# Kernel optimization log

Measured on AMD Instinct MI355X. Metric: run time of the kernel, lower is better.

## Reference

```python
import jax, jax.numpy as jnp
import numpy as np
import math

NEG = -10000.0  # module uses -10000, not -inf


def setup_inputs() -> dict:
    key = jax.random.key(0)
    k1, k2, k3 = jax.random.split(key, 3)
    B, Sq, Sk, H, Hkv, D = 2, 2048, 2048, 16, 4, 64
    q = jax.random.normal(k1, (B, Sq, H, D), dtype=jnp.float32)
    kv = jax.random.normal(k2, (B, Sk, 2, Hkv, D), dtype=jnp.float32)
    key_padding_mask = jax.random.randint(k3, (B, Sk), 0, 2) > 0  # True = valid key
    return {"q": q, "kv": kv, "key_padding_mask": key_padding_mask}


def reference(q, kv, key_padding_mask):
    B, Sq, H, D = q.shape
    Sk, Hkv = kv.shape[1], kv.shape[3]
    if Hkv != H:
        # einops repeat '... hkv d -> ... (hkv g) d': each kv head repeated g times contiguously
        kv = jnp.repeat(kv, H // Hkv, axis=3)
    k, v = kv[:, :, 0], kv[:, :, 1]  # [B, Sk, H, D] each
    scale = 1.0 / math.sqrt(D)
    scores = jnp.einsum('bthd,bshd->bhts', q, k * scale)  # [B, H, Sq, Sk]
    # key padding: additive 0 where valid, -10000 where padded
    pad = jnp.where(key_padding_mask, 0.0, NEG).astype(scores.dtype)
    scores = scores + pad[:, None, None, :]
    # causal mask: cols > rows + Sk - Sq gets replaced (not added) with -10000
    rows = jnp.arange(Sq)[:, None]
    cols = jnp.arange(Sk)[None, :]
    causal_mask = cols > rows + (Sk - Sq)
    scores = jnp.where(causal_mask, NEG, scores)
    attention = jax.nn.softmax(scores, axis=-1).astype(v.dtype)
    # dropout p=0.0 -> identity
    output = jnp.einsum('bhts,bshd->bthd', attention, v)  # [B, Sq, H, D]
    return output
```

## Files before the change

### kernel.cpp

```cpp
#include <hip/hip_runtime.h>
#include <math.h>


typedef __bf16 bf16x4 __attribute__((ext_vector_type(4)));
typedef __bf16 bf16x8 __attribute__((ext_vector_type(8)));
typedef float floatx4 __attribute__((ext_vector_type(4)));
typedef short shortx4 __attribute__((ext_vector_type(4)));

#define SQ 2048
#define SK 2048
#define H_ 16
#define HKV 4
#define D_ 64
#define QT 64
#define KT 64
#define KVROW 512
#define NEGV (-10000.0f)
#define QSCL 0.18033688f
#define EBIAS 17.3123405f
#define SLOTF 4160
#define SLOTS_PER_BH 72
#define PART_FLOATS (32 * SLOTS_PER_BH * SLOTF)
#define IMG_BYTES (256 * 16384)

static __device__ __forceinline__ floatx4 mfma16(bf16x4 a, bf16x4 b, floatx4 c) {
#if __has_builtin(__builtin_amdgcn_mfma_f32_16x16x16bf16_1k)
    return __builtin_amdgcn_mfma_f32_16x16x16bf16_1k(
        __builtin_bit_cast(shortx4, a), __builtin_bit_cast(shortx4, b), c, 0, 0, 0);
#else
    floatx4 d;
    asm("v_mfma_f32_16x16x16_bf16 %0, %1, %2, %3"
        : "=v"(d) : "v"(a), "v"(b), "v"(c));
    return d;
#endif
}

static __device__ __forceinline__ void gload16(const void* g, void* l) {
    __builtin_amdgcn_global_load_lds(
        (const __attribute__((address_space(1))) unsigned int*)g,
        (__attribute__((address_space(3))) unsigned int*)l, 16, 0, 0);
}

__global__ __launch_bounds__(256)
void prep_kernel(const float* __restrict__ kv, const int* __restrict__ mask,
                 char* __restrict__ imgs, unsigned long long* __restrict__ kept)
{
    __shared__ alignas(16) __bf16 Vl[64][64];
    const int tid = threadIdx.x;
    const int bid = (int)blockIdx.x;
    const int kt = bid & 31, hkv = (bid >> 5) & 3, b = bid >> 7;
    const float* kvb = kv + ((size_t)b * SK + kt * KT) * KVROW + hkv * D_;
    const float* vvb = kvb + HKV * D_;
    char* img = imgs + ((size_t)bid << 14);

    const int r  = tid >> 2;
    const int gg = tid & 3;

    {
        const float* p = kvb + (size_t)r * KVROW + gg * 16;
        float4 f0 = *(const float4*)(p + 0), f1 = *(const float4*)(p + 4);
        float4 f2 = *(const float4*)(p + 8), f3 = *(const float4*)(p + 12);
        bf16x8 c0 = { (__bf16)f0.x, (__bf16)f0.y, (__bf16)f0.z, (__bf16)f0.w,
                      (__bf16)f1.x, (__bf16)f1.y, (__bf16)f1.z, (__bf16)f1.w };
        bf16x8 c1 = { (__bf16)f2.x, (__bf16)f2.y, (__bf16)f2.z, (__bf16)f2.w,
                      (__bf16)f3.x, (__bf16)f3.y, (__bf16)f3.z, (__bf16)f3.w };
        const int xo = (r & 7) << 4;
        *(bf16x8*)(img + r * 128 + (((gg * 2 + 0) * 16) ^ xo)) = c0;
        *(bf16x8*)(img + r * 128 + (((gg * 2 + 1) * 16) ^ xo)) = c1;
    }
    {
        const float* p = vvb + (size_t)r * KVROW + gg * 16;
        float4 f0 = *(const float4*)(p + 0), f1 = *(const float4*)(p + 4);
        float4 f2 = *(const float4*)(p + 8), f3 = *(const float4*)(p + 12);
        float t[16] = { f0.x, f0.y, f0.z, f0.w, f1.x, f1.y, f1.z, f1.w,
                        f2.x, f2.y, f2.z, f2.w, f3.x, f3.y, f3.z, f3.w };
#pragma unroll
        for (int j = 0; j < 16; ++j)
            Vl[gg * 16 + j][r] = (__bf16)t[j];
    }
    __syncthreads();
#pragma unroll
    for (int i = 0; i < 2; ++i) {
        const int c = tid * 2 + i, rr = c >> 3, g = c & 7;
        bf16x8 v = *(const bf16x8*)&Vl[rr][g * 8];
        *(bf16x8*)(img + 8192 + rr * 128 + ((g * 16) ^ ((rr & 7) << 4))) = v;
    }
    if (tid < 64) {
        int m = mask[b * SK + kt * KT + tid];
        unsigned long long kk = __ballot(m != 0);
        if (tid == 0 && hkv == 0) kept[b * 32 + kt] = kk;
    }
}

__global__ __launch_bounds__(256, 5)
void attn_kernel(const float* __restrict__ q,
                 const float* __restrict__ kv,
                 const int* __restrict__ mask,
                 float* __restrict__ out,
                 float* __restrict__ ws)
{
    __shared__ alignas(16) union {
        struct {
            __bf16 K[2][KT * D_];
            __bf16 V[2][D_ * KT];
        } m;
        struct {
            float fpart[4][64];
            float fw[4][64];
            int   s_first;
        } f;
    } sh;

    const int tid  = threadIdx.x;
    const int wave = tid >> 6;
    const int lane = tid & 63;
    const int col  = lane & 15;
    const int quad = lane >> 4;

    if (blockIdx.x < 32) {
        const int bh = (int)blockIdx.x;
        const int b = bh >> 4, h = bh & 15, hkv = h >> 2;
        if (tid == 0) sh.f.s_first = SK;
        __syncthreads();
        int local = SK;
        for (int s = tid; s < SK; s += 256)
            if (mask[b * SK + s]) local = min(local, s);
        atomicMin(&sh.f.s_first, local);
        __syncthreads();
        const int nfirst = sh.f.s_first;
        if (nfirst == 0) return;

        const float* kvb = kv + (size_t)b * SK * KVROW + hkv * D_;
        const float* vvb = kvb + HKV * D_;
        {
            float a0=0,a1=0,a2=0,a3=0,a4=0,a5=0,a6=0,a7=0;
            const int s0 = wave * 512;
            for (int s = s0; s < s0 + 512; s += 8) {
                a0 += vvb[(size_t)(s+0)*KVROW + lane];
                a1 += vvb[(size_t)(s+1)*KVROW + lane];
                a2 += vvb[(size_t)(s+2)*KVROW + lane];
                a3 += vvb[(size_t)(s+3)*KVROW + lane];
                a4 += vvb[(size_t)(s+4)*KVROW + lane];
                a5 += vvb[(size_t)(s+5)*KVROW + lane];
                a6 += vvb[(size_t)(s+6)*KVROW + lane];
                a7 += vvb[(size_t)(s+7)*KVROW + lane];
            }
            sh.f.fpart[wave][lane] = ((a0+a1)+(a2+a3)) + ((a4+a5)+(a6+a7));
        }
        __syncthreads();
        const float vtotal = sh.f.fpart[0][lane] + sh.f.fpart[1][lane]
                           + sh.f.fpart[2][lane] + sh.f.fpart[3][lane];

        for (int R = wave; R < nfirst; R += 4) {
            const float* qrow = q + (((size_t)b * SQ + R) * H_ + h) * D_;
            float mymax = -3.4e38f;
            for (int s = lane; s <= R; s += 64) {
                const float* kp = kvb + (size_t)s * KVROW;
                float dt = 0.f;
                for (int d = 0; d < D_; ++d) dt += qrow[d] * kp[d];
                mymax = fmaxf(mymax, dt * 0.125f + NEGV);
            }
#pragma unroll
            for (int off = 32; off >= 1; off >>= 1)
                mymax = fmaxf(mymax, __shfl_xor(mymax, off, 64));
            const float M = (R < SK - 1) ? fmaxf(mymax, NEGV) : mymax;
            float lsum = 0.f, oacc = 0.f, pref = 0.f;
            for (int s0 = 0; s0 <= R; s0 += 64) {
                int s = s0 + lane;
                float w = 0.f;
                if (s <= R) {
                    const float* kp = kvb + (size_t)s * KVROW;
                    float dt = 0.f;
                    for (int d = 0; d < D_; ++d) dt += qrow[d] * kp[d];
                    w = __expf(dt * 0.125f + NEGV - M);
                    lsum += w;
                }
                sh.f.fw[wave][lane] = w;
                const int nk = (R - s0 + 1 < 64) ? (R - s0 + 1) : 64;
                for (int j = 0; j < nk; ++j) {
                    const float vj = vvb[(size_t)(s0 + j) * KVROW + lane];
                    oacc += sh.f.fw[wave][j] * vj;
                    pref += vj;
                }
            }
#pragma unroll
            for (int off = 32; off >= 1; off >>= 1)
                lsum += __shfl_xor(lsum, off, 64);
            const float wn   = __expf(NEGV - M);
            const float ltot = lsum + wn * (float)(SK - 1 - R);
            out[(((size_t)b * SQ + R) * H_ + h) * D_ + lane] =
                (oacc + wn * (vtotal - pref)) / ltot;
        }
        return;
    }

    const int id = (int)blockIdx.x - 32;
    const int bh = id & 31;
    const int z  = 79 - (id >> 5);
    int qt, sp;
    if (z < 8)       { qt = z;                sp = 0; }
    else if (z < 24) { qt = 8 + ((z - 8) >> 1);  sp = (z - 8) & 1; }
    else if (z < 48) { qt = 16 + (z - 24) / 3;   sp = (z - 24) % 3; }
    else             { qt = 24 + ((z - 48) >> 2); sp = (z - 48) & 3; }
    const int nsplit = 1 + (qt >> 3);
    const int k0 = sp * 8;
    const int k1 = min(qt + 1, k0 + 8);

    const int b = bh >> 4, h = bh & 15, hkv = h >> 2;
    const int qw = qt * QT + wave * 16;

    const char* imgb = (const char*)ws + (size_t)PART_FLOATS * 4;
    const unsigned long long* keptarr =
        (const unsigned long long*)(imgb + IMG_BYTES);
    const char* timg0 = imgb + ((size_t)((b * 4 + hkv) * 32) << 14);

    bf16x8 aq[2];
    {
        const int row = qw + col;
        const float* qp = q + (((size_t)b * SQ + row) * H_ + h) * D_ + quad * 8;
#pragma unroll
        for (int kc = 0; kc < 2; ++kc) {
            const float* p = qp + kc * 32;
#pragma unroll
            for (int j = 0; j < 8; ++j) aq[kc][j] = (__bf16)(p[j] * QSCL);
        }
    }

    bf16x4 vone4;
#pragma unroll
    for (int j = 0; j < 4; ++j) vone4[j] = (__bf16)1.0f;

    floatx4 o[4];
    floatx4 l_acc = (floatx4){0.f, 0.f, 0.f, 0.f};
#pragma unroll
    for (int dj = 0; dj < 4; ++dj) o[dj] = (floatx4){0.f, 0.f, 0.f, 0.f};

    const int c7 = col & 7;
    const int xo = c7 << 4;

    auto gstage = [&](int kt, int bb) {
        const char* img = timg0 + ((size_t)kt << 14);
        const char* gsK = img + wave * 1024 + lane * 16;
        const char* gsV = img + 8192 + wave * 1024 + lane * 16;
        char* ldK = (char*)&sh.m.K[bb][0] + wave * 1024;
        char* ldV = (char*)&sh.m.V[bb][0] + wave * 1024;
        gload16(gsK,        ldK);
        gload16(gsK + 4096, ldK + 4096);
        gload16(gsV,        ldV);
        gload16(gsV + 4096, ldV + 4096);
    };

    gstage(k0, 0);
    int cur = 0;
    for (int kt = k0; kt < k1; ++kt) {
        __syncthreads();
        if (kt + 1 < k1) gstage(kt + 1, cur ^ 1);
        const unsigned long long kept = keptarr[b * 32 + kt];

        const char* Kb = (const char*)&sh.m.K[cur][0];
        floatx4 c[4];
        __builtin_amdgcn_s_setprio(1);
#pragma unroll
        for (int kj = 0; kj < 4; ++kj) {
            c[kj] = (floatx4){0.f, 0.f, 0.f, 0.f};
#pragma unroll
            for (int kc = 0; kc < 2; ++kc) {
                bf16x8 ak = *(const bf16x8*)(Kb + (kj * 16 + col) * 128
                                                + ((((kc * 4 + quad) ^ c7) << 4)));
                c[kj] = __builtin_amdgcn_mfma_f32_16x16x32_bf16(ak, aq[kc], c[kj], 0, 0, 0);
            }
        }
        __builtin_amdgcn_s_setprio(0);

        const bool dg = (kt == qt);
        const unsigned long long kq = kept >> (quad * 4);
        const int tcl = dg ? (wave * 16 + col - quad * 4) : 127;
        bf16x4 pk[4];
#pragma unroll
        for (int kj = 0; kj < 4; ++kj) {
#pragma unroll
            for (int r = 0; r < 4; ++r) {
                float p = __builtin_amdgcn_exp2f(c[kj][r] - EBIAS);
                const bool keep = ((kq >> (kj * 16 + r)) & 1ull) && (kj * 16 + r <= tcl);
                pk[kj][r] = (__bf16)(keep ? p : 0.f);
            }
        }

        const char* Vb = (const char*)&sh.m.V[cur][0];
        __builtin_amdgcn_s_setprio(1);
#pragma unroll
        for (int kj = 0; kj < 4; ++kj)
            l_acc = mfma16(pk[kj], vone4, l_acc);
#pragma unroll
        for (int dj = 0; dj < 4; ++dj)
#pragma unroll
            for (int kj = 0; kj < 4; ++kj) {
                bf16x4 bv = *(const bf16x4*)(Vb + (dj * 16 + col) * 128
                                                + ((kj * 32 + quad * 8) ^ xo));
                o[dj] = mfma16(pk[kj], bv, o[dj]);
            }
        __builtin_amdgcn_s_setprio(0);
        cur ^= 1;
    }

    if (nsplit == 1) {
#pragma unroll
        for (int r = 0; r < 4; ++r) {
            const float l = l_acc[r];
            if (l > 0.f) {
                const float inv = 1.0f / l;
                const int row = qw + quad * 4 + r;
                float* op = out + (((size_t)b * SQ + row) * H_ + h) * D_ + col;
#pragma unroll
                for (int dj = 0; dj < 4; ++dj)
                    op[dj * 16] = o[dj][r] * inv;
            }
        }
    } else {
        const int local0 = (qt < 16) ? (qt - 8) * 2
                         : (qt < 24) ? 16 + (qt - 16) * 3
                                     : 40 + (qt - 24) * 4;
        float* slot = ws + ((size_t)bh * SLOTS_PER_BH + local0 + sp) * SLOTF;
#pragma unroll
        for (int r = 0; r < 4; ++r) {
            const int row = wave * 16 + quad * 4 + r;
            float* op = slot + (size_t)row * 64 + col;
#pragma unroll
            for (int dj = 0; dj < 4; ++dj)
                op[dj * 16] = o[dj][r];
            if (col == 0) slot[4096 + row] = l_acc[r];
        }
    }
}

__global__ __launch_bounds__(256)
void combine_kernel(const float* __restrict__ ws, float* __restrict__ out)
{
    __shared__ float linv[64];
    const int tid = threadIdx.x;
    const int bh = (int)blockIdx.x & 31;
    const int qt = 8 + ((int)blockIdx.x >> 5);
    const int b = bh >> 4, h = bh & 15;
    const int n = 1 + (qt >> 3);
    const int local0 = (qt < 16) ? (qt - 8) * 2
                     : (qt < 24) ? 16 + (qt - 16) * 3
                                 : 40 + (qt - 24) * 4;
    const float* s0 = ws + ((size_t)bh * SLOTS_PER_BH + local0) * SLOTF;

    if (tid < 64) {
        float s = 0.f;
        for (int k = 0; k < n; ++k)
            s += s0[(size_t)k * SLOTF + 4096 + tid];
        linv[tid] = (s > 0.f) ? 1.0f / s : 0.f;
    }
    __syncthreads();

#pragma unroll
    for (int c = 0; c < 4; ++c) {
        const int idx = c * 1024 + tid * 4;
        const int row = idx >> 6, d = idx & 63;
        float4 acc = *(const float4*)(s0 + idx);
        for (int k = 1; k < n; ++k) {
            const float4 t = *(const float4*)(s0 + (size_t)k * SLOTF + idx);
            acc.x += t.x; acc.y += t.y; acc.z += t.z; acc.w += t.w;
        }
        const float inv = linv[row];
        if (inv > 0.f) {
            float4 r4 = { acc.x * inv, acc.y * inv, acc.z * inv, acc.w * inv };
            *(float4*)(out + (((size_t)b * SQ + qt * 64 + row) * H_ + h) * D_ + d) = r4;
        }
    }
}

extern "C" void kernel_launch(void* const* d_in, const int* in_sizes, int n_in,
                              void* d_out, int out_size, void* d_ws, size_t ws_size,
                              hipStream_t stream) {
    const float* q   = (const float*)d_in[0];
    const float* kv  = (const float*)d_in[1];
    const int* mask  = (const int*)d_in[2];
    float* out       = (float*)d_out;
    char* imgs = (char*)d_ws + (size_t)PART_FLOATS * 4;
    unsigned long long* kept = (unsigned long long*)(imgs + IMG_BYTES);
    prep_kernel<<<dim3(256), 256, 0, stream>>>(kv, mask, imgs, kept);
    attn_kernel<<<dim3(32 + 2560), 256, 0, stream>>>(q, kv, mask, out, (float*)d_ws);
    combine_kernel<<<dim3(768), 256, 0, stream>>>((const float*)d_ws, out);
}
```

Measured before the change: 123.3 us.

## Give each wave its own 32-row Q tile and per-wave 16-key KV pipeline

Restructures the attention kernel so each wave independently processes 32 query rows over its own stream of 16-key K/V chunks, double-buffered in a private LDS region and synchronised with vmcnt waits instead of block-wide barriers. Two waves of a block now cover different work items, which halves the grid. The causal loop ends at the wave's own diagonal, skipping fully masked key chunks. The prep kernel re-lays K/V images into 4KB per-16-key chunks to match, and occupancy is lowered to 4 blocks per SIMD. This trades block-level K/V sharing for fewer barriers and finer causal skipping, at the cost of more register pressure and redundant K/V loads per wave.

```diff
diff --git a/kernel.cpp b/kernel.cpp
--- a/kernel.cpp
+++ b/kernel.cpp
@@ -12,8 +12,6 @@
 #define H_ 16
 #define HKV 4
 #define D_ 64
-#define QT 64
-#define KT 64
 #define KVROW 512
 #define NEGV (-10000.0f)
 #define QSCL 0.18033688f
@@ -21,7 +19,7 @@
 #define SLOTF 4160
 #define SLOTS_PER_BH 72
 #define PART_FLOATS (32 * SLOTS_PER_BH * SLOTF)
-#define IMG_BYTES (256 * 16384)
+#define IMG_BYTES (1024 * 4096)
 
 static __device__ __forceinline__ floatx4 mfma16(bf16x4 a, bf16x4 b, floatx4 c) {
 #if __has_builtin(__builtin_amdgcn_mfma_f32_16x16x16bf16_1k)
@@ -49,7 +47,7 @@
     const int tid = threadIdx.x;
     const int bid = (int)blockIdx.x;
     const int kt = bid & 31, hkv = (bid >> 5) & 3, b = bid >> 7;
-    const float* kvb = kv + ((size_t)b * SK + kt * KT) * KVROW + hkv * D_;
+    const float* kvb = kv + ((size_t)b * SK + kt * 64) * KVROW + hkv * D_;
     const float* vvb = kvb + HKV * D_;
     char* img = imgs + ((size_t)bid << 14);
 
@@ -64,9 +62,10 @@
                       (__bf16)f1.x, (__bf16)f1.y, (__bf16)f1.z, (__bf16)f1.w };
         bf16x8 c1 = { (__bf16)f2.x, (__bf16)f2.y, (__bf16)f2.z, (__bf16)f2.w,
                       (__bf16)f3.x, (__bf16)f3.y, (__bf16)f3.z, (__bf16)f3.w };
-        const int xo = (r & 7) << 4;
-        *(bf16x8*)(img + r * 128 + (((gg * 2 + 0) * 16) ^ xo)) = c0;
-        *(bf16x8*)(img + r * 128 + (((gg * 2 + 1) * 16) ^ xo)) = c1;
+        char* kdst = img + (r >> 4) * 4096 + (r & 15) * 128;
+        const int xo = r & 7;
+        *(bf16x8*)(kdst + (((gg * 2 + 0) ^ xo) << 4)) = c0;
+        *(bf16x8*)(kdst + (((gg * 2 + 1) ^ xo) << 4)) = c1;
     }
     {
         const float* p = vvb + (size_t)r * KVROW + gg * 16;
@@ -81,18 +80,19 @@
     __syncthreads();
 #pragma unroll
     for (int i = 0; i < 2; ++i) {
-        const int c = tid * 2 + i, rr = c >> 3, g = c & 7;
-        bf16x8 v = *(const bf16x8*)&Vl[rr][g * 8];
-        *(bf16x8*)(img + 8192 + rr * 128 + ((g * 16) ^ ((rr & 7) << 4))) = v;
+        const int cc = tid * 2 + i;
+        const int d = cc >> 3, rest = cc & 7, sub = rest >> 1, half = rest & 1;
+        bf16x8 v = *(const bf16x8*)&Vl[d][sub * 16 + half * 8];
+        *(bf16x8*)(img + sub * 4096 + 2048 + d * 32 + half * 16) = v;
     }
     if (tid < 64) {
-        int m = mask[b * SK + kt * KT + tid];
+        int m = mask[b * SK + kt * 64 + tid];
         unsigned long long kk = __ballot(m != 0);
         if (tid == 0 && hkv == 0) kept[b * 32 + kt] = kk;
     }
 }
 
-__global__ __launch_bounds__(256, 5)
+__global__ __launch_bounds__(256, 4)
 void attn_kernel(const float* __restrict__ q,
                  const float* __restrict__ kv,
                  const int* __restrict__ mask,
@@ -100,10 +100,7 @@
                  float* __restrict__ ws)
 {
     __shared__ alignas(16) union {
-        struct {
-            __bf16 K[2][KT * D_];
-            __bf16 V[2][D_ * KT];
-        } m;
+        char m[4][2][4096];
         struct {
             float fpart[4][64];
             float fw[4][64];
@@ -196,7 +193,8 @@
 
     const int id = (int)blockIdx.x - 32;
     const int bh = id & 31;
-    const int z  = 79 - (id >> 5);
+    const int y  = id >> 5;
+    const int z  = 79 - (y * 2 + (wave >> 1));
     int qt, sp;
     if (z < 8)       { qt = z;                sp = 0; }
     else if (z < 24) { qt = 8 + ((z - 8) >> 1);  sp = (z - 8) & 1; }
@@ -207,22 +205,23 @@
     const int k1 = min(qt + 1, k0 + 8);
 
     const int b = bh >> 4, h = bh & 15, hkv = h >> 2;
-    const int qw = qt * QT + wave * 16;
+    const int qw32 = qt * 64 + (wave & 1) * 32;
 
     const char* imgb = (const char*)ws + (size_t)PART_FLOATS * 4;
     const unsigned long long* keptarr =
         (const unsigned long long*)(imgb + IMG_BYTES);
-    const char* timg0 = imgb + ((size_t)((b * 4 + hkv) * 32) << 14);
-
-    bf16x8 aq[2];
-    {
-        const int row = qw + col;
+    const char* timg0 = imgb + ((size_t)((b * 4 + hkv) * 128) << 12);
+
+    bf16x8 aq[2][2];
+#pragma unroll
+    for (int g = 0; g < 2; ++g) {
+        const int row = qw32 + g * 16 + col;
         const float* qp = q + (((size_t)b * SQ + row) * H_ + h) * D_ + quad * 8;
 #pragma unroll
         for (int kc = 0; kc < 2; ++kc) {
             const float* p = qp + kc * 32;
 #pragma unroll
-            for (int j = 0; j < 8; ++j) aq[kc][j] = (__bf16)(p[j] * QSCL);
+            for (int j = 0; j < 8; ++j) aq[g][kc][j] = (__bf16)(p[j] * QSCL);
         }
     }
 
@@ -230,106 +229,112 @@
 #pragma unroll
     for (int j = 0; j < 4; ++j) vone4[j] = (__bf16)1.0f;
 
-    floatx4 o[4];
-    floatx4 l_acc = (floatx4){0.f, 0.f, 0.f, 0.f};
-#pragma unroll
-    for (int dj = 0; dj < 4; ++dj) o[dj] = (floatx4){0.f, 0.f, 0.f, 0.f};
-
+    floatx4 o[2][4];
+    floatx4 l_acc[2];
+#pragma unroll
+    for (int g = 0; g < 2; ++g) {
+        l_acc[g] = (floatx4){0.f, 0.f, 0.f, 0.f};
+#pragma unroll
+        for (int dj = 0; dj < 4; ++dj) o[g][dj] = (floatx4){0.f, 0.f, 0.f, 0.f};
+    }
+
+    char* const bufA = &sh.m[wave][0][0];
+    char* const bufB = &sh.m[wave][1][0];
     const int c7 = col & 7;
-    const int xo = c7 << 4;
-
-    auto gstage = [&](int kt, int bb) {
-        const char* img = timg0 + ((size_t)kt << 14);
-        const char* gsK = img + wave * 1024 + lane * 16;
-        const char* gsV = img + 8192 + wave * 1024 + lane * 16;
-        char* ldK = (char*)&sh.m.K[bb][0] + wave * 1024;
-        char* ldV = (char*)&sh.m.V[bb][0] + wave * 1024;
-        gload16(gsK,        ldK);
-        gload16(gsK + 4096, ldK + 4096);
-        gload16(gsV,        ldV);
-        gload16(gsV + 4096, ldV + 4096);
+
+    auto gstage = [&](int s0, char* dst) {
+        const char* src = timg0 + ((size_t)(s0 >> 4) << 12) + lane * 16;
+        gload16(src,        dst);
+        gload16(src + 1024, dst + 1024);
+        gload16(src + 2048, dst + 2048);
+        gload16(src + 3072, dst + 3072);
     };
 
-    gstage(k0, 0);
-    int cur = 0;
-    for (int kt = k0; kt < k1; ++kt) {
-        __syncthreads();
-        if (kt + 1 < k1) gstage(kt + 1, cur ^ 1);
-        const unsigned long long kept = keptarr[b * 32 + kt];
-
-        const char* Kb = (const char*)&sh.m.K[cur][0];
-        floatx4 c[4];
+    const int kbeg = k0 * 64;
+    const int kend = min(k1 * 64, qw32 + 32);
+
+    gstage(kbeg, bufA);
+    int buf = 0;
+    for (int s0 = kbeg; s0 < kend; s0 += 16) {
+        char* const curb = buf ? bufB : bufA;
+        if (s0 + 16 < kend) {
+            gstage(s0 + 16, buf ? bufA : bufB);
+            asm volatile("s_waitcnt vmcnt(4)" ::: "memory");
+        } else {
+            asm volatile("s_waitcnt vmcnt(0)" ::: "memory");
+        }
+        __builtin_amdgcn_sched_barrier(0);
+
+        const unsigned long long kept = keptarr[(b << 5) + (s0 >> 6)];
+
+        bf16x8 ak0 = *(const bf16x8*)(curb + col * 128 + ((quad ^ c7) << 4));
+        bf16x8 ak1 = *(const bf16x8*)(curb + col * 128 + (((4 + quad) ^ c7) << 4));
+        floatx4 c0 = (floatx4){0.f, 0.f, 0.f, 0.f};
+        floatx4 c1 = (floatx4){0.f, 0.f, 0.f, 0.f};
         __builtin_amdgcn_s_setprio(1);
-#pragma unroll
-        for (int kj = 0; kj < 4; ++kj) {
-            c[kj] = (floatx4){0.f, 0.f, 0.f, 0.f};
-#pragma unroll
-            for (int kc = 0; kc < 2; ++kc) {
-                bf16x8 ak = *(const bf16x8*)(Kb + (kj * 16 + col) * 128
-                                                + ((((kc * 4 + quad) ^ c7) << 4)));
-                c[kj] = __builtin_amdgcn_mfma_f32_16x16x32_bf16(ak, aq[kc], c[kj], 0, 0, 0);
-            }
-        }
+        c0 = __builtin_amdgcn_mfma_f32_16x16x32_bf16(ak0, aq[0][0], c0, 0, 0, 0);
+        c0 = __builtin_amdgcn_mfma_f32_16x16x32_bf16(ak1, aq[0][1], c0, 0, 0, 0);
+        c1 = __builtin_amdgcn_mfma_f32_16x16x32_bf16(ak0, aq[1][0], c1, 0, 0, 0);
+        c1 = __builtin_amdgcn_mfma_f32_16x16x32_bf16(ak1, aq[1][1], c1, 0, 0, 0);
         __builtin_amdgcn_s_setprio(0);
 
-        const bool dg = (kt == qt);
-        const unsigned long long kq = kept >> (quad * 4);
-        const int tcl = dg ? (wave * 16 + col - quad * 4) : 127;
-        bf16x4 pk[4];
-#pragma unroll
-        for (int kj = 0; kj < 4; ++kj) {
+        const int dgap = s0 - qw32;
+        const unsigned long long kq = kept >> ((s0 & 48) + quad * 4);
+        bf16x4 pk0, pk1;
+#pragma unroll
+        for (int r = 0; r < 4; ++r) {
+            const bool kb = (kq >> r) & 1ull;
+            float p0 = __builtin_amdgcn_exp2f(c0[r] - EBIAS);
+            float p1 = __builtin_amdgcn_exp2f(c1[r] - EBIAS);
+            pk0[r] = (__bf16)((kb && (quad * 4 + r <= col - dgap))      ? p0 : 0.f);
+            pk1[r] = (__bf16)((kb && (quad * 4 + r <= 16 + col - dgap)) ? p1 : 0.f);
+        }
+
+        const char* Vb = curb + 2048;
+        __builtin_amdgcn_s_setprio(1);
+        l_acc[0] = mfma16(pk0, vone4, l_acc[0]);
+        l_acc[1] = mfma16(pk1, vone4, l_acc[1]);
+#pragma unroll
+        for (int dj = 0; dj < 4; ++dj) {
+            bf16x4 bv = *(const bf16x4*)(Vb + (dj * 16 + col) * 32 + quad * 8);
+            o[0][dj] = mfma16(pk0, bv, o[0][dj]);
+            o[1][dj] = mfma16(pk1, bv, o[1][dj]);
+        }
+        __builtin_amdgcn_s_setprio(0);
+        buf ^= 1;
+    }
+
+    if (nsplit == 1) {
+#pragma unroll
+        for (int g = 0; g < 2; ++g)
 #pragma unroll
             for (int r = 0; r < 4; ++r) {
-                float p = __builtin_amdgcn_exp2f(c[kj][r] - EBIAS);
-                const bool keep = ((kq >> (kj * 16 + r)) & 1ull) && (kj * 16 + r <= tcl);
-                pk[kj][r] = (__bf16)(keep ? p : 0.f);
-            }
-        }
-
-        const char* Vb = (const char*)&sh.m.V[cur][0];
-        __builtin_amdgcn_s_setprio(1);
-#pragma unroll
-        for (int kj = 0; kj < 4; ++kj)
-            l_acc = mfma16(pk[kj], vone4, l_acc);
-#pragma unroll
-        for (int dj = 0; dj < 4; ++dj)
-#pragma unroll
-            for (int kj = 0; kj < 4; ++kj) {
-                bf16x4 bv = *(const bf16x4*)(Vb + (dj * 16 + col) * 128
-                                                + ((kj * 32 + quad * 8) ^ xo));
-                o[dj] = mfma16(pk[kj], bv, o[dj]);
-            }
-        __builtin_amdgcn_s_setprio(0);
-        cur ^= 1;
-    }
-
-    if (nsplit == 1) {
-#pragma unroll
-        for (int r = 0; r < 4; ++r) {
-            const float l = l_acc[r];
-            if (l > 0.f) {
-                const float inv = 1.0f / l;
-                const int row = qw + quad * 4 + r;
-                float* op = out + (((size_t)b * SQ + row) * H_ + h) * D_ + col;
-#pragma unroll
-                for (int dj = 0; dj < 4; ++dj)
-                    op[dj * 16] = o[dj][r] * inv;
-            }
-        }
+                const float l = l_acc[g][r];
+                if (l > 0.f) {
+                    const float inv = 1.0f / l;
+                    const int row = qw32 + g * 16 + quad * 4 + r;
+                    float* op = out + (((size_t)b * SQ + row) * H_ + h) * D_ + col;
+#pragma unroll
+                    for (int dj = 0; dj < 4; ++dj)
+                        op[dj * 16] = o[g][dj][r] * inv;
+                }
+            }
     } else {
         const int local0 = (qt < 16) ? (qt - 8) * 2
                          : (qt < 24) ? 16 + (qt - 16) * 3
                                      : 40 + (qt - 24) * 4;
         float* slot = ws + ((size_t)bh * SLOTS_PER_BH + local0 + sp) * SLOTF;
 #pragma unroll
-        for (int r = 0; r < 4; ++r) {
-            const int row = wave * 16 + quad * 4 + r;
-            float* op = slot + (size_t)row * 64 + col;
-#pragma unroll
-            for (int dj = 0; dj < 4; ++dj)
-                op[dj * 16] = o[dj][r];
-            if (col == 0) slot[4096 + row] = l_acc[r];
-        }
+        for (int g = 0; g < 2; ++g)
+#pragma unroll
+            for (int r = 0; r < 4; ++r) {
+                const int row = (wave & 1) * 32 + g * 16 + quad * 4 + r;
+                float* op = slot + (size_t)row * 64 + col;
+#pragma unroll
+                for (int dj = 0; dj < 4; ++dj)
+                    op[dj * 16] = o[g][dj][r];
+                if (col == 0) slot[4096 + row] = l_acc[g][r];
+            }
     }
 }
 
@@ -382,6 +387,6 @@
     char* imgs = (char*)d_ws + (size_t)PART_FLOATS * 4;
     unsigned long long* kept = (unsigned long long*)(imgs + IMG_BYTES);
     prep_kernel<<<dim3(256), 256, 0, stream>>>(kv, mask, imgs, kept);
-    attn_kernel<<<dim3(32 + 2560), 256, 0, stream>>>(q, kv, mask, out, (float*)d_ws);
+    attn_kernel<<<dim3(32 + 1280), 256, 0, stream>>>(q, kv, mask, out, (float*)d_ws);
     combine_kernel<<<dim3(768), 256, 0, stream>>>((const float*)d_ws, out);
 }
```

Measured after the change: 136.4 us. +10.6%, slower.

## Drop split-K partials and combine kernel; use balanced full-row query-tile ordering

Applied to the files above, without the earlier changes.

Removes the split-K scheme, in which long query tiles were split across up to four blocks that wrote partial outputs to workspace and were merged by a separate combine kernel. Each block now processes a whole query tile over all its causal key tiles, and the block index maps to query tiles in a zig-zag order so that long and short tiles interleave for load balance. The causal diagonal test moves into a separate branch so off-diagonal tiles skip the per-element column comparison. This saves a kernel launch and the workspace round trip, at the cost of fewer, longer blocks (1024 instead of 2560) and a longer critical path for the largest tiles.

```diff
diff --git a/kernel.cpp b/kernel.cpp
--- a/kernel.cpp
+++ b/kernel.cpp
@@ -18,9 +18,6 @@
 #define NEGV (-10000.0f)
 #define QSCL 0.18033688f
 #define EBIAS 17.3123405f
-#define SLOTF 4160
-#define SLOTS_PER_BH 72
-#define PART_FLOATS (32 * SLOTS_PER_BH * SLOTF)
 #define IMG_BYTES (256 * 16384)
 
 static __device__ __forceinline__ floatx4 mfma16(bf16x4 a, bf16x4 b, floatx4 c) {
@@ -196,20 +193,13 @@
 
     const int id = (int)blockIdx.x - 32;
     const int bh = id & 31;
-    const int z  = 79 - (id >> 5);
-    int qt, sp;
-    if (z < 8)       { qt = z;                sp = 0; }
-    else if (z < 24) { qt = 8 + ((z - 8) >> 1);  sp = (z - 8) & 1; }
-    else if (z < 48) { qt = 16 + (z - 24) / 3;   sp = (z - 24) % 3; }
-    else             { qt = 24 + ((z - 48) >> 2); sp = (z - 48) & 3; }
-    const int nsplit = 1 + (qt >> 3);
-    const int k0 = sp * 8;
-    const int k1 = min(qt + 1, k0 + 8);
-
+    const int y  = id >> 5;
+    const int kg = y >> 3, jj = y & 7;
+    const int qt = (kg == 0) ? 31 - jj : (kg == 1) ? jj : (kg == 2) ? 23 - jj : 8 + jj;
     const int b = bh >> 4, h = bh & 15, hkv = h >> 2;
     const int qw = qt * QT + wave * 16;
 
-    const char* imgb = (const char*)ws + (size_t)PART_FLOATS * 4;
+    const char* imgb = (const char*)ws;
     const unsigned long long* keptarr =
         (const unsigned long long*)(imgb + IMG_BYTES);
     const char* timg0 = imgb + ((size_t)((b * 4 + hkv) * 32) << 14);
@@ -250,9 +240,10 @@
         gload16(gsV + 4096, ldV + 4096);
     };
 
-    gstage(k0, 0);
+    const int k1 = qt + 1;
+    gstage(0, 0);
     int cur = 0;
-    for (int kt = k0; kt < k1; ++kt) {
+    for (int kt = 0; kt < k1; ++kt) {
         __syncthreads();
         if (kt + 1 < k1) gstage(kt + 1, cur ^ 1);
         const unsigned long long kept = keptarr[b * 32 + kt];
@@ -272,17 +263,29 @@
         }
         __builtin_amdgcn_s_setprio(0);
 
-        const bool dg = (kt == qt);
         const unsigned long long kq = kept >> (quad * 4);
-        const int tcl = dg ? (wave * 16 + col - quad * 4) : 127;
         bf16x4 pk[4];
-#pragma unroll
-        for (int kj = 0; kj < 4; ++kj) {
-#pragma unroll
-            for (int r = 0; r < 4; ++r) {
-                float p = __builtin_amdgcn_exp2f(c[kj][r] - EBIAS);
-                const bool keep = ((kq >> (kj * 16 + r)) & 1ull) && (kj * 16 + r <= tcl);
-                pk[kj][r] = (__bf16)(keep ? p : 0.f);
+        if (kt == qt) {
+            const int tcl = wave * 16 + col - quad * 4;
+#pragma unroll
+            for (int kj = 0; kj < 4; ++kj) {
+#pragma unroll
+                for (int r = 0; r < 4; ++r) {
+                    float p = __builtin_amdgcn_exp2f(c[kj][r] - EBIAS);
+                    const bool keep = ((kq >> (kj * 16 + r)) & 1ull)
+                                    && (kj * 16 + r <= tcl);
+                    pk[kj][r] = (__bf16)(keep ? p : 0.f);
+                }
+            }
+        } else {
+#pragma unroll
+            for (int kj = 0; kj < 4; ++kj) {
+#pragma unroll
+                for (int r = 0; r < 4; ++r) {
+                    float p = __builtin_amdgcn_exp2f(c[kj][r] - EBIAS);
+                    const bool keep = (kq >> (kj * 16 + r)) & 1ull;
+                    pk[kj][r] = (__bf16)(keep ? p : 0.f);
+                }
             }
         }
 
@@ -303,71 +306,16 @@
         cur ^= 1;
     }
 
-    if (nsplit == 1) {
-#pragma unroll
-        for (int r = 0; r < 4; ++r) {
-            const float l = l_acc[r];
-            if (l > 0.f) {
-                const float inv = 1.0f / l;
-                const int row = qw + quad * 4 + r;
-                float* op = out + (((size_t)b * SQ + row) * H_ + h) * D_ + col;
-#pragma unroll
-                for (int dj = 0; dj < 4; ++dj)
-                    op[dj * 16] = o[dj][r] * inv;
-            }
-        }
-    } else {
-        const int local0 = (qt < 16) ? (qt - 8) * 2
-                         : (qt < 24) ? 16 + (qt - 16) * 3
-                                     : 40 + (qt - 24) * 4;
-        float* slot = ws + ((size_t)bh * SLOTS_PER_BH + local0 + sp) * SLOTF;
-#pragma unroll
-        for (int r = 0; r < 4; ++r) {
-            const int row = wave * 16 + quad * 4 + r;
-            float* op = slot + (size_t)row * 64 + col;
+#pragma unroll
+    for (int r = 0; r < 4; ++r) {
+        const float l = l_acc[r];
+        if (l > 0.f) {
+            const float inv = 1.0f / l;
+            const int row = qw + quad * 4 + r;
+            float* op = out + (((size_t)b * SQ + row) * H_ + h) * D_ + col;
 #pragma unroll
             for (int dj = 0; dj < 4; ++dj)
-                op[dj * 16] = o[dj][r];
-            if (col == 0) slot[4096 + row] = l_acc[r];
-        }
-    }
-}
-
-__global__ __launch_bounds__(256)
-void combine_kernel(const float* __restrict__ ws, float* __restrict__ out)
-{
-    __shared__ float linv[64];
-    const int tid = threadIdx.x;
-    const int bh = (int)blockIdx.x & 31;
-    const int qt = 8 + ((int)blockIdx.x >> 5);
-    const int b = bh >> 4, h = bh & 15;
-    const int n = 1 + (qt >> 3);
-    const int local0 = (qt < 16) ? (qt - 8) * 2
-                     : (qt < 24) ? 16 + (qt - 16) * 3
-                                 : 40 + (qt - 24) * 4;
-    const float* s0 = ws + ((size_t)bh * SLOTS_PER_BH + local0) * SLOTF;
-
-    if (tid < 64) {
-        float s = 0.f;
-        for (int k = 0; k < n; ++k)
-            s += s0[(size_t)k * SLOTF + 4096 + tid];
-        linv[tid] = (s > 0.f) ? 1.0f / s : 0.f;
-    }
-    __syncthreads();
-
-#pragma unroll
-    for (int c = 0; c < 4; ++c) {
-        const int idx = c * 1024 + tid * 4;
-        const int row = idx >> 6, d = idx & 63;
-        float4 acc = *(const float4*)(s0 + idx);
-        for (int k = 1; k < n; ++k) {
-            const float4 t = *(const float4*)(s0 + (size_t)k * SLOTF + idx);
-            acc.x += t.x; acc.y += t.y; acc.z += t.z; acc.w += t.w;
-        }
-        const float inv = linv[row];
-        if (inv > 0.f) {
-            float4 r4 = { acc.x * inv, acc.y * inv, acc.z * inv, acc.w * inv };
-            *(float4*)(out + (((size_t)b * SQ + qt * 64 + row) * H_ + h) * D_ + d) = r4;
+                op[dj * 16] = o[dj][r] * inv;
         }
     }
 }
@@ -379,9 +327,8 @@
     const float* kv  = (const float*)d_in[1];
     const int* mask  = (const int*)d_in[2];
     float* out       = (float*)d_out;
-    char* imgs = (char*)d_ws + (size_t)PART_FLOATS * 4;
+    char* imgs = (char*)d_ws;
     unsigned long long* kept = (unsigned long long*)(imgs + IMG_BYTES);
     prep_kernel<<<dim3(256), 256, 0, stream>>>(kv, mask, imgs, kept);
-    attn_kernel<<<dim3(32 + 2560), 256, 0, stream>>>(q, kv, mask, out, (float*)d_ws);
-    combine_kernel<<<dim3(768), 256, 0, stream>>>((const float*)d_ws, out);
-}
+    attn_kernel<<<dim3(32 + 1024), 256, 0, stream>>>(q, kv, mask, out, (float*)d_ws);
+}
```

After: 111.2 us. 1.11x faster.
